# Performance work log

Hardware: AMD Instinct MI355X
Metric: run time of the kernel (lower is better)

The kernel has to match this reference:

```python
import jax, jax.numpy as jnp
import numpy as np

M = 128  # split point: first M units use max-plus, rest use min-plus

def setup_inputs() -> dict:
    key = jax.random.key(0)
    k1, k2 = jax.random.split(key)
    x = jax.random.normal(k1, (2048, 512), dtype=jnp.float32)   # (batch, features_in)
    w = jax.random.normal(k2, (512, 256), dtype=jnp.float32)    # (features_in, units)
    return {"x": x, "w": w}

def reference(x, w):
    # Tropical (max/min-plus) pseudo-matmul.
    # s[b, f, u] = x[b, f] + w[f, u]; reduce over f.
    s_max = x[:, :, None] + w[None, :, :M]          # (batch, f, M)
    s_min = x[:, :, None] + w[None, :, M:]          # (batch, f, units-M)
    hv = jnp.max(s_max, axis=1)                     # (batch, M)
    hw = jnp.min(s_min, axis=1)                     # (batch, units-M)
    return jnp.concatenate([hv, hw], axis=1)        # linear activation = identity
```

## Files before the change

kernel.cpp:

```cpp
#include <hip/hip_runtime.h>
#include <math.h>


#define FEAT  512
#define UNITS 256
#define TM    8
#define KW    64

template<bool IS_MAX>
__device__ __forceinline__ void trop_body(const float* __restrict__ x,
                                          const float* __restrict__ w,
                                          float* __restrict__ out,
                                          int ubase, float* __restrict__ part) {
    const int tid  = threadIdx.x;
    const int lane = tid & 63;
    const int wv   = __builtin_amdgcn_readfirstlane(tid >> 6);
    const int u    = ubase + lane;
    const int row0 = blockIdx.y * TM;
    const int kbase = wv * KW;

    float acc[TM];
    #pragma unroll
    for (int r = 0; r < TM; ++r) acc[r] = IS_MAX ? -__builtin_inff() : __builtin_inff();

    const float* wp = w + (size_t)kbase * UNITS + u;
    const float* xp = x + kbase;

    #pragma unroll
    for (int i = 0; i < KW / 8; ++i) {
        const int k0 = i * 8;
        const float wk0 = wp[(k0 + 0) * UNITS];
        const float wk1 = wp[(k0 + 1) * UNITS];
        const float wk2 = wp[(k0 + 2) * UNITS];
        const float wk3 = wp[(k0 + 3) * UNITS];
        const float wk4 = wp[(k0 + 4) * UNITS];
        const float wk5 = wp[(k0 + 5) * UNITS];
        const float wk6 = wp[(k0 + 6) * UNITS];
        const float wk7 = wp[(k0 + 7) * UNITS];

        #pragma unroll
        for (int r = 0; r < TM; ++r) {
            const float4* xr = (const float4*)(xp + (size_t)(row0 + r) * FEAT + k0);
            const float4 a0 = xr[0];
            const float4 a1 = xr[1];

            const float s0 = a0.x + wk0, s1 = a0.y + wk1;
            const float s2 = a0.z + wk2, s3 = a0.w + wk3;
            const float s4 = a1.x + wk4, s5 = a1.y + wk5;
            const float s6 = a1.z + wk6, s7 = a1.w + wk7;

            if (IS_MAX) {
                const float m0 = fmaxf(fmaxf(s0, s1), s2);
                const float m1 = fmaxf(fmaxf(s3, s4), s5);
                const float m2 = fmaxf(fmaxf(s6, s7), acc[r]);
                acc[r] = fmaxf(fmaxf(m0, m1), m2);
            } else {
                const float m0 = fminf(fminf(s0, s1), s2);
                const float m1 = fminf(fminf(s3, s4), s5);
                const float m2 = fminf(fminf(s6, s7), acc[r]);
                acc[r] = fminf(fminf(m0, m1), m2);
            }
        }
    }

    #pragma unroll
    for (int r = 0; r < TM; ++r)
        part[(wv * TM + r) * 64 + lane] = acc[r];
    __syncthreads();

    const int r = tid >> 6;
    float v = part[r * 64 + lane];
    #pragma unroll
    for (int j = 1; j < 8; ++j) {
        const float p = part[(j * TM + r) * 64 + lane];
        v = IS_MAX ? fmaxf(v, p) : fminf(v, p);
    }
    out[(size_t)(row0 + r) * UNITS + u] = v;
}

__global__ __launch_bounds__(512, 8) void tropical_kernel(const float* __restrict__ x,
                                                          const float* __restrict__ w,
                                                          float* __restrict__ out) {
    __shared__ float part[8 * TM * 64];
    const int ubase = blockIdx.x * 64;
    if (ubase < 128) trop_body<true>(x, w, out, ubase, part);
    else             trop_body<false>(x, w, out, ubase, part);
}

extern "C" void kernel_launch(void* const* d_in, const int* in_sizes, int n_in,
                              void* d_out, int out_size, void* d_ws, size_t ws_size,
                              hipStream_t stream) {
    const float* x = (const float*)d_in[0];
    const float* w = (const float*)d_in[1];
    float* out = (float*)d_out;

    dim3 grid(UNITS / 64, 2048 / TM);
    tropical_kernel<<<grid, dim3(512), 0, stream>>>(x, w, out);
}
```

Baseline: 74.91 us.

## Compute two units per thread with float2 weights and double-buffered weight loads

Each thread now computes two adjacent output units using float2 weight loads, which halves the grid in the unit dimension and reuses every x load across two columns. Weight rows for the next octet are prefetched into a second register buffer while the current octet is computed, and the partial reduction through shared memory is widened to float2. This raises register pressure and lowers the occupancy hint, and it halves the number of blocks.

New measurement: 76.01 us. Within noise of the previous version (+1.5%).

```diff
diff --git a/kernel.cpp b/kernel.cpp
--- a/kernel.cpp
+++ b/kernel.cpp
@@ -4,8 +4,35 @@
 
 #define FEAT  512
 #define UNITS 256
-#define TM    8
+#define R     8
 #define KW    64
+#define NW    8
+
+template<bool IS_MAX>
+__device__ __forceinline__ float tmerge(float a, float b) {
+    return IS_MAX ? fmaxf(a, b) : fminf(a, b);
+}
+
+template<bool IS_MAX>
+__device__ __forceinline__ void oct_compute(const float* __restrict__ xp, int oct,
+                                            const float2* __restrict__ wb,
+                                            float2* __restrict__ acc) {
+    #pragma unroll
+    for (int r = 0; r < R; ++r) {
+        const float4 a0 = *(const float4*)(xp + (size_t)r * FEAT + oct * 8);
+        const float4 a1 = *(const float4*)(xp + (size_t)r * FEAT + oct * 8 + 4);
+        float2 A = acc[r];
+        A.x = tmerge<IS_MAX>(tmerge<IS_MAX>(A.x, a0.x + wb[0].x), a0.y + wb[1].x);
+        A.x = tmerge<IS_MAX>(tmerge<IS_MAX>(A.x, a0.z + wb[2].x), a0.w + wb[3].x);
+        A.x = tmerge<IS_MAX>(tmerge<IS_MAX>(A.x, a1.x + wb[4].x), a1.y + wb[5].x);
+        A.x = tmerge<IS_MAX>(tmerge<IS_MAX>(A.x, a1.z + wb[6].x), a1.w + wb[7].x);
+        A.y = tmerge<IS_MAX>(tmerge<IS_MAX>(A.y, a0.x + wb[0].y), a0.y + wb[1].y);
+        A.y = tmerge<IS_MAX>(tmerge<IS_MAX>(A.y, a0.z + wb[2].y), a0.w + wb[3].y);
+        A.y = tmerge<IS_MAX>(tmerge<IS_MAX>(A.y, a1.x + wb[4].y), a1.y + wb[5].y);
+        A.y = tmerge<IS_MAX>(tmerge<IS_MAX>(A.y, a1.z + wb[6].y), a1.w + wb[7].y);
+        acc[r] = A;
+    }
+}
 
 template<bool IS_MAX>
 __device__ __forceinline__ void trop_body(const float* __restrict__ x,
@@ -15,74 +42,56 @@
     const int tid  = threadIdx.x;
     const int lane = tid & 63;
     const int wv   = __builtin_amdgcn_readfirstlane(tid >> 6);
-    const int u    = ubase + lane;
-    const int row0 = blockIdx.y * TM;
-    const int kbase = wv * KW;
+    const int u    = ubase + lane * 2;
+    const int row0 = blockIdx.y * R;
+    const int kb   = wv * KW;
 
-    float acc[TM];
+    const float* wp = w + (size_t)kb * UNITS + u;
+    const float* xp = x + (size_t)row0 * FEAT + kb;
+
+    float2 acc[R];
+    const float init = IS_MAX ? -__builtin_inff() : __builtin_inff();
     #pragma unroll
-    for (int r = 0; r < TM; ++r) acc[r] = IS_MAX ? -__builtin_inff() : __builtin_inff();
+    for (int r = 0; r < R; ++r) acc[r] = make_float2(init, init);
 
-    const float* wp = w + (size_t)kbase * UNITS + u;
-    const float* xp = x + kbase;
+    float2 wA[8], wB[8];
+    #pragma unroll
+    for (int k = 0; k < 8; ++k) wA[k] = *(const float2*)(wp + (size_t)k * UNITS);
 
     #pragma unroll
-    for (int i = 0; i < KW / 8; ++i) {
-        const int k0 = i * 8;
-        const float wk0 = wp[(k0 + 0) * UNITS];
-        const float wk1 = wp[(k0 + 1) * UNITS];
-        const float wk2 = wp[(k0 + 2) * UNITS];
-        const float wk3 = wp[(k0 + 3) * UNITS];
-        const float wk4 = wp[(k0 + 4) * UNITS];
-        const float wk5 = wp[(k0 + 5) * UNITS];
-        const float wk6 = wp[(k0 + 6) * UNITS];
-        const float wk7 = wp[(k0 + 7) * UNITS];
-
+    for (int oct = 0; oct < KW / 8; oct += 2) {
         #pragma unroll
-        for (int r = 0; r < TM; ++r) {
-            const float4* xr = (const float4*)(xp + (size_t)(row0 + r) * FEAT + k0);
-            const float4 a0 = xr[0];
-            const float4 a1 = xr[1];
-
-            const float s0 = a0.x + wk0, s1 = a0.y + wk1;
-            const float s2 = a0.z + wk2, s3 = a0.w + wk3;
-            const float s4 = a1.x + wk4, s5 = a1.y + wk5;
-            const float s6 = a1.z + wk6, s7 = a1.w + wk7;
-
-            if (IS_MAX) {
-                const float m0 = fmaxf(fmaxf(s0, s1), s2);
-                const float m1 = fmaxf(fmaxf(s3, s4), s5);
-                const float m2 = fmaxf(fmaxf(s6, s7), acc[r]);
-                acc[r] = fmaxf(fmaxf(m0, m1), m2);
-            } else {
-                const float m0 = fminf(fminf(s0, s1), s2);
-                const float m1 = fminf(fminf(s3, s4), s5);
-                const float m2 = fminf(fminf(s6, s7), acc[r]);
-                acc[r] = fminf(fminf(m0, m1), m2);
-            }
+        for (int k = 0; k < 8; ++k)
+            wB[k] = *(const float2*)(wp + (size_t)((oct + 1) * 8 + k) * UNITS);
+        oct_compute<IS_MAX>(xp, oct, wA, acc);
+        if (oct + 2 < KW / 8) {
+            #pragma unroll
+            for (int k = 0; k < 8; ++k)
+                wA[k] = *(const float2*)(wp + (size_t)((oct + 2) * 8 + k) * UNITS);
         }
+        oct_compute<IS_MAX>(xp, oct + 1, wB, acc);
     }
 
     #pragma unroll
-    for (int r = 0; r < TM; ++r)
-        part[(wv * TM + r) * 64 + lane] = acc[r];
+    for (int r = 0; r < R; ++r)
+        *(float2*)&part[(wv * R + r) * 128 + lane * 2] = acc[r];
     __syncthreads();
 
-    const int r = tid >> 6;
-    float v = part[r * 64 + lane];
+    float2 v = *(const float2*)&part[(size_t)(0 * R + wv) * 128 + lane * 2];
     #pragma unroll
-    for (int j = 1; j < 8; ++j) {
-        const float p = part[(j * TM + r) * 64 + lane];
-        v = IS_MAX ? fmaxf(v, p) : fminf(v, p);
+    for (int j = 1; j < NW; ++j) {
+        const float2 p = *(const float2*)&part[(size_t)(j * R + wv) * 128 + lane * 2];
+        v.x = tmerge<IS_MAX>(v.x, p.x);
+        v.y = tmerge<IS_MAX>(v.y, p.y);
     }
-    out[(size_t)(row0 + r) * UNITS + u] = v;
+    *(float2*)&out[(size_t)(row0 + wv) * UNITS + u] = v;
 }
 
-__global__ __launch_bounds__(512, 8) void tropical_kernel(const float* __restrict__ x,
+__global__ __launch_bounds__(512, 4) void tropical_kernel(const float* __restrict__ x,
                                                           const float* __restrict__ w,
                                                           float* __restrict__ out) {
-    __shared__ float part[8 * TM * 64];
-    const int ubase = blockIdx.x * 64;
+    __shared__ float part[NW * R * 128];
+    const int ubase = blockIdx.x * 128;
     if (ubase < 128) trop_body<true>(x, w, out, ubase, part);
     else             trop_body<false>(x, w, out, ubase, part);
 }
@@ -94,6 +103,6 @@
     const float* w = (const float*)d_in[1];
     float* out = (float*)d_out;
 
-    dim3 grid(UNITS / 64, 2048 / TM);
+    dim3 grid(UNITS / 128, 2048 / R);
     tropical_kernel<<<grid, dim3(512), 0, stream>>>(x, w, out);
 }
```
